# Kernel optimization log

Hardware: AMD Instinct MI355X
Metric: run time of the kernel (lower is better)

## Reference

```python
import jax, jax.numpy as jnp
import numpy as np

B, S, D, H = 2, 4096, 512, 8
DK = D // H  # 64

def setup_inputs() -> dict:
    key = jax.random.key(0)
    k1, k2, k3, k4 = jax.random.split(key, 4)
    return {
        "queries": jax.random.normal(k1, (B, S, D), dtype=jnp.float32),
        "keys": jax.random.normal(k2, (B, S, D), dtype=jnp.float32),
        "values": jax.random.normal(k3, (B, S, D), dtype=jnp.float32),
        "W_o": jax.random.normal(k4, (D, D), dtype=jnp.float32) * (1.0 / np.sqrt(D)),
        "b_o": jnp.zeros((D,), dtype=jnp.float32),
    }

def reference(queries, keys, values, W_o, b_o):
    b_s, nq, _ = queries.shape
    nk = keys.shape[1]
    # split heads: (b, s, h, dk) -> (b, h, s, dk)
    q = queries.reshape(b_s, nq, H, DK).transpose(0, 2, 1, 3)
    k = keys.reshape(b_s, nk, H, DK).transpose(0, 2, 1, 3)
    v = values.reshape(b_s, nk, H, DK).transpose(0, 2, 1, 3)
    # full (nq, nk) attention matrix, scaled by sqrt(d_k)
    att = jnp.einsum("bhqd,bhkd->bhqk", q, k) / np.sqrt(DK).astype(np.float32)
    att = jax.nn.softmax(att, axis=-1)  # dropout is identity at inference
    out = jnp.einsum("bhqk,bhkd->bhqd", att, v)
    out = out.transpose(0, 2, 1, 3).reshape(b_s, nq, H * DK)
    return out @ W_o + b_o
```

## Files before the change

### kernel.cpp

```cpp
#include <hip/hip_runtime.h>
#include <hip/hip_bf16.h>

#define Bn 2
#define Sn 4096
#define Dn 512
#define Hn 8

typedef __bf16 bf16x8 __attribute__((ext_vector_type(8)));
typedef float f32x16 __attribute__((ext_vector_type(16)));

static __device__ __forceinline__ unsigned pk2(float a, float b) {
    unsigned ua = __float_as_uint(a) + 0x8000u;
    unsigned ub = __float_as_uint(b) + 0x8000u;
    return __builtin_amdgcn_perm(ub, ua, 0x07060302u);
}

static __device__ __forceinline__ bf16x8 xchg2(unsigned g0x, unsigned g0y,
                                               unsigned g1x, unsigned g1y, int hi) {
    int sx = hi ? (int)g0x : (int)g1x;
    int sy = hi ? (int)g0y : (int)g1y;
    int rx = __shfl_xor(sx, 32);
    int ry = __shfl_xor(sy, 32);
    unsigned ox = hi ? g1x : g0x;
    unsigned oy = hi ? g1y : g0y;
    union { unsigned u[4]; bf16x8 v; } f;
    f.u[0] = hi ? (unsigned)rx : ox;
    f.u[1] = hi ? (unsigned)ry : oy;
    f.u[2] = hi ? ox : (unsigned)rx;
    f.u[3] = hi ? oy : (unsigned)ry;
    return f.v;
}

__global__ __launch_bounds__(256) void prep_kernel(
    const float* __restrict__ K, const float* __restrict__ V, const float* __restrict__ W,
    unsigned short* __restrict__ Kb, unsigned short* __restrict__ Vb,
    unsigned short* __restrict__ Wb) {
    const int vb = blockIdx.x;
    const int tid = threadIdx.x;
    if (vb < 1024) {
        const int kt = vb & 63, bh = vb >> 6;
        const int b = bh >> 3, h = bh & 7;
        unsigned short* dst = Kb + ((size_t)bh * 64 + kt) * 4096;
#pragma unroll
        for (int i = 0; i < 2; ++i) {
            int c = tid + i * 256;
            int f = c >> 6, ln = c & 63;
            int ktile = f >> 2, ks = f & 3;
            int row = ktile * 32 + (ln & 31);
            int dk = ks * 16 + (ln >> 5) * 8;
            const float* src = K + ((size_t)(b * Sn + kt * 64 + row)) * Dn + h * 64 + dk;
            float4 a0 = *(const float4*)src;
            float4 a1 = *(const float4*)(src + 4);
            uint4 o;
            o.x = pk2(a0.x, a0.y); o.y = pk2(a0.z, a0.w);
            o.z = pk2(a1.x, a1.y); o.w = pk2(a1.z, a1.w);
            *(uint4*)(dst + c * 8) = o;
        }
    } else if (vb < 2048) {
        const int u = vb - 1024;
        const int kt = u & 63, bh = u >> 6;
        const int b = bh >> 3, h = bh & 7;
        unsigned short* dst = Vb + ((size_t)bh * 64 + kt) * 4096;
#pragma unroll
        for (int i = 0; i < 2; ++i) {
            int c = tid + i * 256;
            int f = c >> 6, ln = c & 63;
            int dt = f >> 2, ks = f & 3;
            int dk = dt * 32 + (ln & 31);
            int key0 = ks * 16 + (ln >> 5) * 8;
            const float* src = V + ((size_t)(b * Sn + kt * 64 + key0)) * Dn + h * 64 + dk;
            uint4 o;
            o.x = pk2(src[0 * Dn], src[1 * Dn]); o.y = pk2(src[2 * Dn], src[3 * Dn]);
            o.z = pk2(src[4 * Dn], src[5 * Dn]); o.w = pk2(src[6 * Dn], src[7 * Dn]);
            *(uint4*)(dst + c * 8) = o;
        }
    } else {
        int c = (vb - 2048) * 256 + tid;
        int ln = c & 63, f = c >> 6;
        int ntile = f >> 5, ks = f & 31;
        int n = ntile * 32 + (ln & 31);
        int k0 = ks * 16 + (ln >> 5) * 8;
        uint4 o;
        o.x = pk2(W[(size_t)(k0 + 0) * Dn + n], W[(size_t)(k0 + 1) * Dn + n]);
        o.y = pk2(W[(size_t)(k0 + 2) * Dn + n], W[(size_t)(k0 + 3) * Dn + n]);
        o.z = pk2(W[(size_t)(k0 + 4) * Dn + n], W[(size_t)(k0 + 5) * Dn + n]);
        o.w = pk2(W[(size_t)(k0 + 6) * Dn + n], W[(size_t)(k0 + 7) * Dn + n]);
        *(uint4*)(Wb + c * 8) = o;
    }
}

__global__ __launch_bounds__(512, 4) void attn_kernel(
    const float* __restrict__ Q,
    const unsigned short* __restrict__ Kb,
    const unsigned short* __restrict__ Vb,
    unsigned short* __restrict__ ObA) {
    __shared__ __align__(16) unsigned short KV[16384];
    __shared__ float Lsh[4][64];

    const int qt = blockIdx.x;
    const int bh = blockIdx.y;
    const int b = bh >> 3, h = bh & 7;
    const int tid = threadIdx.x;
    const int wg = tid >> 6;
    const int half = wg >> 2;
    const int w4 = wg & 3;
    const int lane = tid & 63;
    const int q = lane & 31;
    const int hi = lane >> 5;
    const int q0 = qt * 128 + w4 * 32;
    const int th = tid & 255;
    const float cexp = 0.18033688f;

    unsigned short* Kbuf = KV + half * 4096;
    unsigned short* Vbuf = KV + 8192 + half * 4096;

    bf16x8 qf[4];
    {
        const float* qp = Q + ((size_t)(b * Sn + q0 + q)) * Dn + h * 64 + hi * 8;
#pragma unroll
        for (int ks = 0; ks < 4; ++ks) {
            float4 a0 = *(const float4*)(qp + ks * 16);
            float4 a1 = *(const float4*)(qp + ks * 16 + 4);
            union { unsigned u[4]; bf16x8 v; } f;
            f.u[0] = pk2(a0.x * cexp, a0.y * cexp);
            f.u[1] = pk2(a0.z * cexp, a0.w * cexp);
            f.u[2] = pk2(a1.x * cexp, a1.y * cexp);
            f.u[3] = pk2(a1.z * cexp, a1.w * cexp);
            qf[ks] = f.v;
        }
    }

    f32x16 zf;
#pragma unroll
    for (int r = 0; r < 16; ++r) zf[r] = 0.f;
    f32x16 oacc[2];
    oacc[0] = zf; oacc[1] = zf;
    float l_ = 0.f;

    const size_t tbase = ((size_t)bh * 64 + half * 32) * 4096;
    const unsigned short* kg = Kb + tbase;
    const unsigned short* vg = Vb + tbase;

    for (int it = 0; it < 32; ++it) {
        __syncthreads();
        {
            const unsigned short* ks_ = kg + (size_t)it * 4096;
            const unsigned short* vs_ = vg + (size_t)it * 4096;
            uint4 k0v = *(const uint4*)(ks_ + th * 8);
            uint4 k1v = *(const uint4*)(ks_ + 2048 + th * 8);
            uint4 v0v = *(const uint4*)(vs_ + th * 8);
            uint4 v1v = *(const uint4*)(vs_ + 2048 + th * 8);
            *(uint4*)&Kbuf[th * 8] = k0v;
            *(uint4*)&Kbuf[2048 + th * 8] = k1v;
            *(uint4*)&Vbuf[th * 8] = v0v;
            *(uint4*)&Vbuf[2048 + th * 8] = v1v;
        }
        __syncthreads();

#pragma unroll
        for (int t = 0; t < 2; ++t) {
            bf16x8 ka = *(const bf16x8*)&Kbuf[(t * 4 + 0) * 512 + lane * 8];
            f32x16 sa = __builtin_amdgcn_mfma_f32_32x32x16_bf16(ka, qf[0], zf, 0, 0, 0);
#pragma unroll
            for (int ks = 1; ks < 4; ++ks) {
                ka = *(const bf16x8*)&Kbuf[(t * 4 + ks) * 512 + lane * 8];
                sa = __builtin_amdgcn_mfma_f32_32x32x16_bf16(ka, qf[ks], sa, 0, 0, 0);
            }
            float e[16];
            float s0 = 0.f, s1 = 0.f;
#pragma unroll
            for (int r = 0; r < 16; r += 2) {
                e[r] = __builtin_amdgcn_exp2f(sa[r]);
                e[r + 1] = __builtin_amdgcn_exp2f(sa[r + 1]);
                s0 += e[r]; s1 += e[r + 1];
            }
            l_ += s0 + s1;
#pragma unroll
            for (int k2 = 0; k2 < 2; ++k2) {
                unsigned g0x = pk2(e[8 * k2 + 0], e[8 * k2 + 1]);
                unsigned g0y = pk2(e[8 * k2 + 2], e[8 * k2 + 3]);
                unsigned g1x = pk2(e[8 * k2 + 4], e[8 * k2 + 5]);
                unsigned g1y = pk2(e[8 * k2 + 6], e[8 * k2 + 7]);
                bf16x8 pb = xchg2(g0x, g0y, g1x, g1y, hi);
                const int kp = t * 2 + k2;
                bf16x8 va0 = *(const bf16x8*)&Vbuf[(0 * 4 + kp) * 512 + lane * 8];
                bf16x8 va1 = *(const bf16x8*)&Vbuf[(1 * 4 + kp) * 512 + lane * 8];
                oacc[0] = __builtin_amdgcn_mfma_f32_32x32x16_bf16(va0, pb, oacc[0], 0, 0, 0);
                oacc[1] = __builtin_amdgcn_mfma_f32_32x32x16_bf16(va1, pb, oacc[1], 0, 0, 0);
            }
        }
    }

    __syncthreads();
    float* rp = (float*)KV + w4 * 2048;
    if (half) {
#pragma unroll
        for (int g = 0; g < 8; ++g) {
            float4 v;
            v.x = oacc[g >> 2][(g & 3) * 4 + 0];
            v.y = oacc[g >> 2][(g & 3) * 4 + 1];
            v.z = oacc[g >> 2][(g & 3) * 4 + 2];
            v.w = oacc[g >> 2][(g & 3) * 4 + 3];
            *(float4*)&rp[g * 256 + lane * 4] = v;
        }
        Lsh[w4][lane] = l_;
    }
    __syncthreads();
    if (!half) {
#pragma unroll
        for (int g = 0; g < 8; ++g) {
            float4 v = *(const float4*)&rp[g * 256 + lane * 4];
            oacc[g >> 2][(g & 3) * 4 + 0] += v.x;
            oacc[g >> 2][(g & 3) * 4 + 1] += v.y;
            oacc[g >> 2][(g & 3) * 4 + 2] += v.z;
            oacc[g >> 2][(g & 3) * 4 + 3] += v.w;
        }
        l_ += Lsh[w4][lane];
        l_ += __shfl_xor(l_, 32);
        const float li = 1.f / l_;
        const int gm = b * 128 + qt * 4 + w4;
#pragma unroll
        for (int ksg = 0; ksg < 4; ++ksg) {
            const int dt = ksg >> 1, k2 = ksg & 1;
            unsigned g0x = pk2(oacc[dt][8 * k2 + 0] * li, oacc[dt][8 * k2 + 1] * li);
            unsigned g0y = pk2(oacc[dt][8 * k2 + 2] * li, oacc[dt][8 * k2 + 3] * li);
            unsigned g1x = pk2(oacc[dt][8 * k2 + 4] * li, oacc[dt][8 * k2 + 5] * li);
            unsigned g1y = pk2(oacc[dt][8 * k2 + 6] * li, oacc[dt][8 * k2 + 7] * li);
            bf16x8 frag = xchg2(g0x, g0y, g1x, g1y, hi);
            union { bf16x8 v; uint4 u; } fu; fu.v = frag;
            *(uint4*)&ObA[((size_t)(gm * 32 + h * 4 + ksg) * 64 + lane) * 8] = fu.u;
        }
    }
}

__global__ __launch_bounds__(256) void proj_kernel(
    const unsigned short* __restrict__ ObA,
    const unsigned short* __restrict__ Wb,
    const float* __restrict__ bias,
    float* __restrict__ out) {
    __shared__ __align__(16) unsigned short Ash[8192];
    __shared__ __align__(16) unsigned short Wsh[4096];

    const int mt = blockIdx.x;
    const int nt = blockIdx.y;
    const int tid = threadIdx.x;
    const int w = tid >> 6;
    const int lane = tid & 63;
    const int q = lane & 31;
    const int hi = lane >> 5;

    f32x16 acc[2];
#pragma unroll
    for (int t = 0; t < 2; ++t)
#pragma unroll
        for (int r = 0; r < 16; ++r) acc[t][r] = 0.f;

    for (int kt = 0; kt < 8; ++kt) {
        __syncthreads();
#pragma unroll
        for (int i = 0; i < 4; ++i) {
            int ci = (tid >> 6) + i * 4;
            int ml = ci >> 2, ksl = ci & 3;
            *(uint4*)&Ash[ci * 512 + lane * 8] =
                *(const uint4*)(ObA + (((size_t)(mt * 4 + ml) * 32 + kt * 4 + ksl) * 64 + lane) * 8);
        }
#pragma unroll
        for (int i = 0; i < 2; ++i) {
            int ci = (tid >> 6) + i * 4;
            int ntl = ci >> 2, ksl = ci & 3;
            *(uint4*)&Wsh[ci * 512 + lane * 8] =
                *(const uint4*)(Wb + (((size_t)(nt * 2 + ntl) * 32 + kt * 4 + ksl) * 64 + lane) * 8);
        }
        __syncthreads();

#pragma unroll
        for (int ks = 0; ks < 4; ++ks) {
            bf16x8 a  = *(const bf16x8*)&Ash[(w * 4 + ks) * 512 + lane * 8];
            bf16x8 b0 = *(const bf16x8*)&Wsh[(0 * 4 + ks) * 512 + lane * 8];
            bf16x8 b1 = *(const bf16x8*)&Wsh[(4 + ks) * 512 + lane * 8];
            acc[0] = __builtin_amdgcn_mfma_f32_32x32x16_bf16(a, b0, acc[0], 0, 0, 0);
            acc[1] = __builtin_amdgcn_mfma_f32_32x32x16_bf16(a, b1, acc[1], 0, 0, 0);
        }
    }

#pragma unroll
    for (int ntl = 0; ntl < 2; ++ntl) {
        int col = nt * 64 + ntl * 32 + q;
        float bv = bias[col];
#pragma unroll
        for (int reg = 0; reg < 16; ++reg) {
            int row = mt * 128 + w * 32 + (reg & 3) + 8 * (reg >> 2) + 4 * hi;
            out[(size_t)row * Dn + col] = acc[ntl][reg] + bv;
        }
    }
}

extern "C" void kernel_launch(void* const* d_in, const int* in_sizes, int n_in,
                              void* d_out, int out_size, void* d_ws, size_t ws_size,
                              hipStream_t stream) {
    const float* Q = (const float*)d_in[0];
    const float* K = (const float*)d_in[1];
    const float* V = (const float*)d_in[2];
    const float* W = (const float*)d_in[3];
    const float* bo = (const float*)d_in[4];
    float* out = (float*)d_out;

    char* ws = (char*)d_ws;
    unsigned short* Kb  = (unsigned short*)(ws);
    unsigned short* Vb  = (unsigned short*)(ws + 8388608);
    unsigned short* Wb  = (unsigned short*)(ws + 16777216);
    unsigned short* ObA = (unsigned short*)(ws + 17301504);

    prep_kernel<<<2176, 256, 0, stream>>>(K, V, W, Kb, Vb, Wb);
    attn_kernel<<<dim3(32, 16), 512, 0, stream>>>(Q, Kb, Vb, ObA);
    proj_kernel<<<dim3(64, 8), 256, 0, stream>>>(ObA, Wb, bo, out);
}
```

Baseline: 193.5 us.

## Switch attention to fp16 MFMA, drop PV lane exchange, prefetch KV tiles in registers

Converts all bf16 paths to fp16 using the packed round-toward-zero convert, and switches the matmuls to the fp16 MFMA variants. The PV product now uses the 32x32x8 fp16 MFMA with a V layout that matches the score accumulator's register layout. This removes the cross-lane shuffle exchange of the exponentials. It also register-prefetches the next K/V tile from global memory during compute. The costs are twice as many PV MFMA instructions and fp16 range risk on exp values and unnormalised sums.

```diff
diff --git a/kernel.cpp b/kernel.cpp
--- a/kernel.cpp
+++ b/kernel.cpp
@@ -6,24 +6,26 @@
 #define Dn 512
 #define Hn 8
 
-typedef __bf16 bf16x8 __attribute__((ext_vector_type(8)));
+typedef _Float16 f16x8 __attribute__((ext_vector_type(8)));
+typedef _Float16 f16x4 __attribute__((ext_vector_type(4)));
+typedef __fp16 fp16x2 __attribute__((ext_vector_type(2)));
 typedef float f32x16 __attribute__((ext_vector_type(16)));
 
-static __device__ __forceinline__ unsigned pk2(float a, float b) {
-    unsigned ua = __float_as_uint(a) + 0x8000u;
-    unsigned ub = __float_as_uint(b) + 0x8000u;
-    return __builtin_amdgcn_perm(ub, ua, 0x07060302u);
-}
-
-static __device__ __forceinline__ bf16x8 xchg2(unsigned g0x, unsigned g0y,
-                                               unsigned g1x, unsigned g1y, int hi) {
+static __device__ __forceinline__ unsigned pkh(float a, float b) {
+    union { fp16x2 h; unsigned u; } r;
+    r.h = __builtin_amdgcn_cvt_pkrtz(a, b);
+    return r.u;
+}
+
+static __device__ __forceinline__ f16x8 xchg2(unsigned g0x, unsigned g0y,
+                                              unsigned g1x, unsigned g1y, int hi) {
     int sx = hi ? (int)g0x : (int)g1x;
     int sy = hi ? (int)g0y : (int)g1y;
     int rx = __shfl_xor(sx, 32);
     int ry = __shfl_xor(sy, 32);
     unsigned ox = hi ? g1x : g0x;
     unsigned oy = hi ? g1y : g0y;
-    union { unsigned u[4]; bf16x8 v; } f;
+    union { unsigned u[4]; f16x8 v; } f;
     f.u[0] = hi ? (unsigned)rx : ox;
     f.u[1] = hi ? (unsigned)ry : oy;
     f.u[2] = hi ? ox : (unsigned)rx;
@@ -52,8 +54,8 @@
             float4 a0 = *(const float4*)src;
             float4 a1 = *(const float4*)(src + 4);
             uint4 o;
-            o.x = pk2(a0.x, a0.y); o.y = pk2(a0.z, a0.w);
-            o.z = pk2(a1.x, a1.y); o.w = pk2(a1.z, a1.w);
+            o.x = pkh(a0.x, a0.y); o.y = pkh(a0.z, a0.w);
+            o.z = pkh(a1.x, a1.y); o.w = pkh(a1.z, a1.w);
             *(uint4*)(dst + c * 8) = o;
         }
     } else if (vb < 2048) {
@@ -62,17 +64,17 @@
         const int b = bh >> 3, h = bh & 7;
         unsigned short* dst = Vb + ((size_t)bh * 64 + kt) * 4096;
 #pragma unroll
-        for (int i = 0; i < 2; ++i) {
+        for (int i = 0; i < 4; ++i) {
             int c = tid + i * 256;
             int f = c >> 6, ln = c & 63;
-            int dt = f >> 2, ks = f & 3;
+            int dt = f >> 3, ks7 = f & 7;
             int dk = dt * 32 + (ln & 31);
-            int key0 = ks * 16 + (ln >> 5) * 8;
+            int key0 = ks7 * 8 + (ln >> 5) * 4;
             const float* src = V + ((size_t)(b * Sn + kt * 64 + key0)) * Dn + h * 64 + dk;
-            uint4 o;
-            o.x = pk2(src[0 * Dn], src[1 * Dn]); o.y = pk2(src[2 * Dn], src[3 * Dn]);
-            o.z = pk2(src[4 * Dn], src[5 * Dn]); o.w = pk2(src[6 * Dn], src[7 * Dn]);
-            *(uint4*)(dst + c * 8) = o;
+            uint2 o;
+            o.x = pkh(src[0 * Dn], src[1 * Dn]);
+            o.y = pkh(src[2 * Dn], src[3 * Dn]);
+            *(uint2*)(dst + c * 4) = o;
         }
     } else {
         int c = (vb - 2048) * 256 + tid;
@@ -81,10 +83,10 @@
         int n = ntile * 32 + (ln & 31);
         int k0 = ks * 16 + (ln >> 5) * 8;
         uint4 o;
-        o.x = pk2(W[(size_t)(k0 + 0) * Dn + n], W[(size_t)(k0 + 1) * Dn + n]);
-        o.y = pk2(W[(size_t)(k0 + 2) * Dn + n], W[(size_t)(k0 + 3) * Dn + n]);
-        o.z = pk2(W[(size_t)(k0 + 4) * Dn + n], W[(size_t)(k0 + 5) * Dn + n]);
-        o.w = pk2(W[(size_t)(k0 + 6) * Dn + n], W[(size_t)(k0 + 7) * Dn + n]);
+        o.x = pkh(W[(size_t)(k0 + 0) * Dn + n], W[(size_t)(k0 + 1) * Dn + n]);
+        o.y = pkh(W[(size_t)(k0 + 2) * Dn + n], W[(size_t)(k0 + 3) * Dn + n]);
+        o.z = pkh(W[(size_t)(k0 + 4) * Dn + n], W[(size_t)(k0 + 5) * Dn + n]);
+        o.w = pkh(W[(size_t)(k0 + 6) * Dn + n], W[(size_t)(k0 + 7) * Dn + n]);
         *(uint4*)(Wb + c * 8) = o;
     }
 }
@@ -114,18 +116,18 @@
     unsigned short* Kbuf = KV + half * 4096;
     unsigned short* Vbuf = KV + 8192 + half * 4096;
 
-    bf16x8 qf[4];
+    f16x8 qf[4];
     {
         const float* qp = Q + ((size_t)(b * Sn + q0 + q)) * Dn + h * 64 + hi * 8;
 #pragma unroll
         for (int ks = 0; ks < 4; ++ks) {
             float4 a0 = *(const float4*)(qp + ks * 16);
             float4 a1 = *(const float4*)(qp + ks * 16 + 4);
-            union { unsigned u[4]; bf16x8 v; } f;
-            f.u[0] = pk2(a0.x * cexp, a0.y * cexp);
-            f.u[1] = pk2(a0.z * cexp, a0.w * cexp);
-            f.u[2] = pk2(a1.x * cexp, a1.y * cexp);
-            f.u[3] = pk2(a1.z * cexp, a1.w * cexp);
+            union { unsigned u[4]; f16x8 v; } f;
+            f.u[0] = pkh(a0.x * cexp, a0.y * cexp);
+            f.u[1] = pkh(a0.z * cexp, a0.w * cexp);
+            f.u[2] = pkh(a1.x * cexp, a1.y * cexp);
+            f.u[3] = pkh(a1.z * cexp, a1.w * cexp);
             qf[ks] = f.v;
         }
     }
@@ -141,30 +143,35 @@
     const unsigned short* kg = Kb + tbase;
     const unsigned short* vg = Vb + tbase;
 
+    uint4 gk0 = *(const uint4*)(kg + th * 16);
+    uint4 gk1 = *(const uint4*)(kg + th * 16 + 8);
+    uint4 gv0 = *(const uint4*)(vg + th * 16);
+    uint4 gv1 = *(const uint4*)(vg + th * 16 + 8);
+
     for (int it = 0; it < 32; ++it) {
         __syncthreads();
-        {
-            const unsigned short* ks_ = kg + (size_t)it * 4096;
-            const unsigned short* vs_ = vg + (size_t)it * 4096;
-            uint4 k0v = *(const uint4*)(ks_ + th * 8);
-            uint4 k1v = *(const uint4*)(ks_ + 2048 + th * 8);
-            uint4 v0v = *(const uint4*)(vs_ + th * 8);
-            uint4 v1v = *(const uint4*)(vs_ + 2048 + th * 8);
-            *(uint4*)&Kbuf[th * 8] = k0v;
-            *(uint4*)&Kbuf[2048 + th * 8] = k1v;
-            *(uint4*)&Vbuf[th * 8] = v0v;
-            *(uint4*)&Vbuf[2048 + th * 8] = v1v;
-        }
+        *(uint4*)&Kbuf[th * 16] = gk0;
+        *(uint4*)&Kbuf[th * 16 + 8] = gk1;
+        *(uint4*)&Vbuf[th * 16] = gv0;
+        *(uint4*)&Vbuf[th * 16 + 8] = gv1;
         __syncthreads();
+        if (it < 31) {
+            const unsigned short* ks_ = kg + (size_t)(it + 1) * 4096;
+            const unsigned short* vs_ = vg + (size_t)(it + 1) * 4096;
+            gk0 = *(const uint4*)(ks_ + th * 16);
+            gk1 = *(const uint4*)(ks_ + th * 16 + 8);
+            gv0 = *(const uint4*)(vs_ + th * 16);
+            gv1 = *(const uint4*)(vs_ + th * 16 + 8);
+        }
 
 #pragma unroll
         for (int t = 0; t < 2; ++t) {
-            bf16x8 ka = *(const bf16x8*)&Kbuf[(t * 4 + 0) * 512 + lane * 8];
-            f32x16 sa = __builtin_amdgcn_mfma_f32_32x32x16_bf16(ka, qf[0], zf, 0, 0, 0);
+            f16x8 ka = *(const f16x8*)&Kbuf[(t * 4 + 0) * 512 + lane * 8];
+            f32x16 sa = __builtin_amdgcn_mfma_f32_32x32x16_f16(ka, qf[0], zf, 0, 0, 0);
 #pragma unroll
             for (int ks = 1; ks < 4; ++ks) {
-                ka = *(const bf16x8*)&Kbuf[(t * 4 + ks) * 512 + lane * 8];
-                sa = __builtin_amdgcn_mfma_f32_32x32x16_bf16(ka, qf[ks], sa, 0, 0, 0);
+                ka = *(const f16x8*)&Kbuf[(t * 4 + ks) * 512 + lane * 8];
+                sa = __builtin_amdgcn_mfma_f32_32x32x16_f16(ka, qf[ks], sa, 0, 0, 0);
             }
             float e[16];
             float s0 = 0.f, s1 = 0.f;
@@ -176,17 +183,14 @@
             }
             l_ += s0 + s1;
 #pragma unroll
-            for (int k2 = 0; k2 < 2; ++k2) {
-                unsigned g0x = pk2(e[8 * k2 + 0], e[8 * k2 + 1]);
-                unsigned g0y = pk2(e[8 * k2 + 2], e[8 * k2 + 3]);
-                unsigned g1x = pk2(e[8 * k2 + 4], e[8 * k2 + 5]);
-                unsigned g1y = pk2(e[8 * k2 + 6], e[8 * k2 + 7]);
-                bf16x8 pb = xchg2(g0x, g0y, g1x, g1y, hi);
-                const int kp = t * 2 + k2;
-                bf16x8 va0 = *(const bf16x8*)&Vbuf[(0 * 4 + kp) * 512 + lane * 8];
-                bf16x8 va1 = *(const bf16x8*)&Vbuf[(1 * 4 + kp) * 512 + lane * 8];
-                oacc[0] = __builtin_amdgcn_mfma_f32_32x32x16_bf16(va0, pb, oacc[0], 0, 0, 0);
-                oacc[1] = __builtin_amdgcn_mfma_f32_32x32x16_bf16(va1, pb, oacc[1], 0, 0, 0);
+            for (int s = 0; s < 4; ++s) {
+                union { unsigned u[2]; f16x4 v; } pb;
+                pb.u[0] = pkh(e[4 * s + 0], e[4 * s + 1]);
+                pb.u[1] = pkh(e[4 * s + 2], e[4 * s + 3]);
+                f16x4 va0 = *(const f16x4*)&Vbuf[(0 * 8 + t * 4 + s) * 256 + lane * 4];
+                f16x4 va1 = *(const f16x4*)&Vbuf[(1 * 8 + t * 4 + s) * 256 + lane * 4];
+                oacc[0] = __builtin_amdgcn_mfma_f32_32x32x8f16(va0, pb.v, oacc[0], 0, 0, 0);
+                oacc[1] = __builtin_amdgcn_mfma_f32_32x32x8f16(va1, pb.v, oacc[1], 0, 0, 0);
             }
         }
     }
@@ -222,12 +226,12 @@
 #pragma unroll
         for (int ksg = 0; ksg < 4; ++ksg) {
             const int dt = ksg >> 1, k2 = ksg & 1;
-            unsigned g0x = pk2(oacc[dt][8 * k2 + 0] * li, oacc[dt][8 * k2 + 1] * li);
-            unsigned g0y = pk2(oacc[dt][8 * k2 + 2] * li, oacc[dt][8 * k2 + 3] * li);
-            unsigned g1x = pk2(oacc[dt][8 * k2 + 4] * li, oacc[dt][8 * k2 + 5] * li);
-            unsigned g1y = pk2(oacc[dt][8 * k2 + 6] * li, oacc[dt][8 * k2 + 7] * li);
-            bf16x8 frag = xchg2(g0x, g0y, g1x, g1y, hi);
-            union { bf16x8 v; uint4 u; } fu; fu.v = frag;
+            unsigned g0x = pkh(oacc[dt][8 * k2 + 0] * li, oacc[dt][8 * k2 + 1] * li);
+            unsigned g0y = pkh(oacc[dt][8 * k2 + 2] * li, oacc[dt][8 * k2 + 3] * li);
+            unsigned g1x = pkh(oacc[dt][8 * k2 + 4] * li, oacc[dt][8 * k2 + 5] * li);
+            unsigned g1y = pkh(oacc[dt][8 * k2 + 6] * li, oacc[dt][8 * k2 + 7] * li);
+            f16x8 frag = xchg2(g0x, g0y, g1x, g1y, hi);
+            union { f16x8 v; uint4 u; } fu; fu.v = frag;
             *(uint4*)&ObA[((size_t)(gm * 32 + h * 4 + ksg) * 64 + lane) * 8] = fu.u;
         }
     }
@@ -275,11 +279,11 @@
 
 #pragma unroll
         for (int ks = 0; ks < 4; ++ks) {
-            bf16x8 a  = *(const bf16x8*)&Ash[(w * 4 + ks) * 512 + lane * 8];
-            bf16x8 b0 = *(const bf16x8*)&Wsh[(0 * 4 + ks) * 512 + lane * 8];
-            bf16x8 b1 = *(const bf16x8*)&Wsh[(4 + ks) * 512 + lane * 8];
-            acc[0] = __builtin_amdgcn_mfma_f32_32x32x16_bf16(a, b0, acc[0], 0, 0, 0);
-            acc[1] = __builtin_amdgcn_mfma_f32_32x32x16_bf16(a, b1, acc[1], 0, 0, 0);
+            f16x8 a  = *(const f16x8*)&Ash[(w * 4 + ks) * 512 + lane * 8];
+            f16x8 b0 = *(const f16x8*)&Wsh[(0 * 4 + ks) * 512 + lane * 8];
+            f16x8 b1 = *(const f16x8*)&Wsh[(4 + ks) * 512 + lane * 8];
+            acc[0] = __builtin_amdgcn_mfma_f32_32x32x16_f16(a, b0, acc[0], 0, 0, 0);
+            acc[1] = __builtin_amdgcn_mfma_f32_32x32x16_f16(a, b1, acc[1], 0, 0, 0);
         }
     }
 
```

After: 190.6 us. No clear change (-1.5%).
